# Performance work log

Measured on AMD Instinct MI355X. Metric: run time of the kernel, lower is better.

Reference implementation:

```python
import jax, jax.numpy as jnp
import numpy as np

B, H, S, Dh = 2, 16, 2048, 64


def setup_inputs() -> dict:
    key = jax.random.key(0)
    kq, kk, kv = jax.random.split(key, 3)
    query = jax.random.normal(kq, (B, H, S, Dh), dtype=jnp.float32)
    k = jax.random.normal(kk, (B, H, S, Dh), dtype=jnp.float32)
    value = jax.random.normal(kv, (B, H, S, Dh), dtype=jnp.float32)
    mask = jnp.zeros((1, 1, S, S), dtype=jnp.float32)
    return {"query": query, "key": k, "value": value, "mask": mask}


def reference(query, key, value, mask):
    # scores: [B,H,S,S]
    dk = jnp.asarray(key.shape[-1], dtype=query.dtype)
    logits = jnp.einsum("bhqd,bhkd->bhqk", query, key) / jnp.sqrt(dk)
    logits = logits + mask * (-1e9)
    attention_weights = jax.nn.softmax(logits, axis=-1)
    output = jnp.einsum("bhqk,bhkd->bhqd", attention_weights, value)
    return (output, attention_weights)
```

## Files before the change

### kernel.cpp

```cpp
#include <hip/hip_runtime.h>
#include <hip/hip_bf16.h>
#include <stdint.h>

typedef __bf16 bf16;
typedef __attribute__((ext_vector_type(8))) __bf16 bf16x8;
typedef __attribute__((ext_vector_type(4))) float f32x4;

constexpr int S   = 2048;
constexpr int DH  = 64;
constexpr int BQ  = 16;
constexpr int LDP = S + 8;

__global__ __launch_bounds__(256, 2)
void attn_fused(const float* __restrict__ Q, const float* __restrict__ K,
                const float* __restrict__ V, const float* __restrict__ Msk,
                float* __restrict__ Out, float* __restrict__ W)
{
    __shared__ bf16  P[BQ][LDP];
    __shared__ float rs[4][BQ];
    __shared__ float inv[BQ];

    const int tid  = threadIdx.x;
    const int lane = tid & 63;
    const int wave = tid >> 6;
    const int c    = lane & 15;
    const int g    = lane >> 4;

    const int swz = (blockIdx.x & 7) * 512 + (blockIdx.x >> 3);
    const int bh = swz >> 7;
    const int q0 = (swz & 127) * BQ;

    const float* Qb = Q + (size_t)bh * S * DH;
    const float* Kb = K + (size_t)bh * S * DH;
    const float* Vb = V + (size_t)bh * S * DH;

    bf16x8 qlo, qhi;
    {
        const float* qr = Qb + (size_t)(q0 + c) * DH + g * 8;
        f32x4 a0 = *(const f32x4*)(qr);
        f32x4 a1 = *(const f32x4*)(qr + 4);
        f32x4 b0 = *(const f32x4*)(qr + 32);
        f32x4 b1 = *(const f32x4*)(qr + 36);
        #pragma unroll
        for (int j = 0; j < 4; ++j) {
            qlo[j]     = (bf16)a0[j];  qlo[j + 4] = (bf16)a1[j];
            qhi[j]     = (bf16)b0[j];  qhi[j + 4] = (bf16)b1[j];
        }
    }

    float sums[4] = {0.f, 0.f, 0.f, 0.f};
    for (int i = 0; i < 16; ++i) {
        const int k0 = (wave * 2 + i * 8) * 16;
        const float* kr0 = Kb + (size_t)(k0 + c) * DH + g * 8;
        const float* kr1 = kr0 + (size_t)16 * DH;
        f32x4 a0 = *(const f32x4*)(kr0);
        f32x4 a1 = *(const f32x4*)(kr0 + 4);
        f32x4 b0 = *(const f32x4*)(kr0 + 32);
        f32x4 b1 = *(const f32x4*)(kr0 + 36);
        f32x4 a2 = *(const f32x4*)(kr1);
        f32x4 a3 = *(const f32x4*)(kr1 + 4);
        f32x4 b2 = *(const f32x4*)(kr1 + 32);
        f32x4 b3 = *(const f32x4*)(kr1 + 36);
        const float* mrow = Msk + (size_t)(q0 + g * 4) * S + k0 + c;
        float m0 = mrow[0], m1 = mrow[S], m2 = mrow[2 * S], m3 = mrow[3 * S];
        float n0 = mrow[16], n1 = mrow[S + 16], n2 = mrow[2 * S + 16], n3 = mrow[3 * S + 16];

        bf16x8 kl0, kh0, kl1, kh1;
        #pragma unroll
        for (int j = 0; j < 4; ++j) {
            kl0[j] = (bf16)a0[j];  kl0[j + 4] = (bf16)a1[j];
            kh0[j] = (bf16)b0[j];  kh0[j + 4] = (bf16)b1[j];
            kl1[j] = (bf16)a2[j];  kl1[j + 4] = (bf16)a3[j];
            kh1[j] = (bf16)b2[j];  kh1[j + 4] = (bf16)b3[j];
        }
        f32x4 acc0 = {0.f, 0.f, 0.f, 0.f};
        f32x4 acc1 = {0.f, 0.f, 0.f, 0.f};
        acc0 = __builtin_amdgcn_mfma_f32_16x16x32_bf16(qlo, kl0, acc0, 0, 0, 0);
        acc0 = __builtin_amdgcn_mfma_f32_16x16x32_bf16(qhi, kh0, acc0, 0, 0, 0);
        acc1 = __builtin_amdgcn_mfma_f32_16x16x32_bf16(qlo, kl1, acc1, 0, 0, 0);
        acc1 = __builtin_amdgcn_mfma_f32_16x16x32_bf16(qhi, kh1, acc1, 0, 0, 0);

        const float mk[4] = {m0, m1, m2, m3};
        const float nk[4] = {n0, n1, n2, n3};
        #pragma unroll
        for (int r = 0; r < 4; ++r) {
            const int row = g * 4 + r;
            const float p0 = __expf(acc0[r] * 0.125f + mk[r] * (-1e9f));
            const float p1 = __expf(acc1[r] * 0.125f + nk[r] * (-1e9f));
            sums[r] += p0 + p1;
            P[row][k0 + c]      = (bf16)p0;
            P[row][k0 + 16 + c] = (bf16)p1;
        }
    }

    #pragma unroll
    for (int r = 0; r < 4; ++r) {
        float s = sums[r];
        s += __shfl_xor(s, 1); s += __shfl_xor(s, 2);
        s += __shfl_xor(s, 4); s += __shfl_xor(s, 8);
        if (c == 0) rs[wave][g * 4 + r] = s;
    }
    __syncthreads();
    if (tid < BQ) inv[tid] = 1.f / (rs[0][tid] + rs[1][tid] + rs[2][tid] + rs[3][tid]);
    __syncthreads();

    float* Wb = W + (size_t)bh * S * S + (size_t)q0 * S;
    #pragma unroll
    for (int it = 0; it < (BQ * S) / (256 * 8); ++it) {
        const int flat = (it * 256 + tid) * 8;
        const int row  = flat >> 11;
        const int col  = flat & (S - 1);
        bf16x8 pv = *(const bf16x8*)&P[row][col];
        const float is = inv[row];
        float* dst = Wb + (size_t)row * S + col;
        f32x4 o0 = { (float)pv[0] * is, (float)pv[1] * is,
                     (float)pv[2] * is, (float)pv[3] * is };
        f32x4 o1 = { (float)pv[4] * is, (float)pv[5] * is,
                     (float)pv[6] * is, (float)pv[7] * is };
        *(f32x4*)(dst)     = o0;
        *(f32x4*)(dst + 4) = o1;
    }

    f32x4 oacc[4] = {{0,0,0,0},{0,0,0,0},{0,0,0,0},{0,0,0,0}};
    const int kbase = wave * (S / 4);
    for (int kc = 0; kc < 16; ++kc) {
        const int kb = kbase + kc * 32;
        bf16x8 pa = *(const bf16x8*)&P[c][kb + g * 8];
        const float* vp = Vb + (size_t)(kb + g * 8) * DH + c;
        float vv0[8], vv1[8], vv2[8], vv3[8];
        #pragma unroll
        for (int j = 0; j < 8; ++j) {
            const float* vr = vp + (size_t)j * DH;
            vv0[j] = vr[0];  vv1[j] = vr[16];
            vv2[j] = vr[32]; vv3[j] = vr[48];
        }
        bf16x8 vb0, vb1, vb2, vb3;
        #pragma unroll
        for (int j = 0; j < 8; ++j) {
            vb0[j] = (bf16)vv0[j]; vb1[j] = (bf16)vv1[j];
            vb2[j] = (bf16)vv2[j]; vb3[j] = (bf16)vv3[j];
        }
        oacc[0] = __builtin_amdgcn_mfma_f32_16x16x32_bf16(pa, vb0, oacc[0], 0, 0, 0);
        oacc[1] = __builtin_amdgcn_mfma_f32_16x16x32_bf16(pa, vb1, oacc[1], 0, 0, 0);
        oacc[2] = __builtin_amdgcn_mfma_f32_16x16x32_bf16(pa, vb2, oacc[2], 0, 0, 0);
        oacc[3] = __builtin_amdgcn_mfma_f32_16x16x32_bf16(pa, vb3, oacc[3], 0, 0, 0);
    }

    __syncthreads();
    float* opart = (float*)&P[0][0];
    #pragma unroll
    for (int d4 = 0; d4 < 4; ++d4)
        #pragma unroll
        for (int r = 0; r < 4; ++r)
            opart[wave * 1024 + (g * 4 + r) * 64 + d4 * 16 + c] = oacc[d4][r];
    __syncthreads();

    {
        const int q = tid >> 4;
        const int d = (tid & 15) * 4;
        const float* p0 = opart + q * 64 + d;
        f32x4 o = *(const f32x4*)(p0)
                + *(const f32x4*)(p0 + 1024)
                + *(const f32x4*)(p0 + 2048)
                + *(const f32x4*)(p0 + 3072);
        const float is = inv[q];
        o.x *= is; o.y *= is; o.z *= is; o.w *= is;
        float* Ob = Out + ((size_t)bh * S + q0 + q) * DH + d;
        *(f32x4*)Ob = o;
    }
}

extern "C" void kernel_launch(void* const* d_in, const int* in_sizes, int n_in,
                              void* d_out, int out_size, void* d_ws, size_t ws_size,
                              hipStream_t stream) {
    const float* Q   = (const float*)d_in[0];
    const float* K   = (const float*)d_in[1];
    const float* V   = (const float*)d_in[2];
    const float* Msk = (const float*)d_in[3];

    float* Out = (float*)d_out;
    float* W   = Out + (size_t)2 * 16 * 2048 * 64;

    dim3 grid(32 * (S / BQ));
    dim3 block(256);
    hipLaunchKernelGGL(attn_fused, grid, block, 0, stream, Q, K, V, Msk, Out, W);
}
```

Baseline: 408.7 us.

## Recompute QK^T in second pass instead of staging probabilities in LDS

Removes the 64KB shared-memory P buffer. The kernel now runs two passes over K: the first computes only the row sums of exp, and the second recomputes the scores, writes normalized weights directly to global memory with nontemporal stores, and feeds the bf16 probabilities straight into the PV MFMA from registers. The MFMA operand order is transposed so each lane holds one query row, which also lets the mask be read with vector loads. Lower LDS use permits higher occupancy (launch bounds raised to 4 blocks), at the cost of reading K twice and redoing the QK MFMAs and exp.

```diff
diff --git a/kernel.cpp b/kernel.cpp
--- a/kernel.cpp
+++ b/kernel.cpp
@@ -6,19 +6,19 @@
 typedef __attribute__((ext_vector_type(8))) __bf16 bf16x8;
 typedef __attribute__((ext_vector_type(4))) float f32x4;
 
-constexpr int S   = 2048;
-constexpr int DH  = 64;
-constexpr int BQ  = 16;
-constexpr int LDP = S + 8;
-
-__global__ __launch_bounds__(256, 2)
+constexpr int S  = 2048;
+constexpr int DH = 64;
+constexpr int BQ = 16;
+
+
+__global__ __launch_bounds__(256, 4)
 void attn_fused(const float* __restrict__ Q, const float* __restrict__ K,
                 const float* __restrict__ V, const float* __restrict__ Msk,
                 float* __restrict__ Out, float* __restrict__ W)
 {
-    __shared__ bf16  P[BQ][LDP];
     __shared__ float rs[4][BQ];
     __shared__ float inv[BQ];
+    __shared__ float opart[4][BQ][DH];
 
     const int tid  = threadIdx.x;
     const int lane = tid & 63;
@@ -48,9 +48,12 @@
         }
     }
 
-    float sums[4] = {0.f, 0.f, 0.f, 0.f};
-    for (int i = 0; i < 16; ++i) {
-        const int k0 = (wave * 2 + i * 8) * 16;
+    const int kbase = wave * (S / 4);
+    const float* mrow = Msk + (size_t)(q0 + c) * S;
+
+    float s = 0.f;
+    for (int kc = 0; kc < 16; ++kc) {
+        const int k0 = kbase + kc * 32;
         const float* kr0 = Kb + (size_t)(k0 + c) * DH + g * 8;
         const float* kr1 = kr0 + (size_t)16 * DH;
         f32x4 a0 = *(const f32x4*)(kr0);
@@ -61,9 +64,8 @@
         f32x4 a3 = *(const f32x4*)(kr1 + 4);
         f32x4 b2 = *(const f32x4*)(kr1 + 32);
         f32x4 b3 = *(const f32x4*)(kr1 + 36);
-        const float* mrow = Msk + (size_t)(q0 + g * 4) * S + k0 + c;
-        float m0 = mrow[0], m1 = mrow[S], m2 = mrow[2 * S], m3 = mrow[3 * S];
-        float n0 = mrow[16], n1 = mrow[S + 16], n2 = mrow[2 * S + 16], n3 = mrow[3 * S + 16];
+        f32x4 m0 = *(const f32x4*)(mrow + k0 + 4 * g);
+        f32x4 m1 = *(const f32x4*)(mrow + k0 + 16 + 4 * g);
 
         bf16x8 kl0, kh0, kl1, kh1;
         #pragma unroll
@@ -75,94 +77,111 @@
         }
         f32x4 acc0 = {0.f, 0.f, 0.f, 0.f};
         f32x4 acc1 = {0.f, 0.f, 0.f, 0.f};
-        acc0 = __builtin_amdgcn_mfma_f32_16x16x32_bf16(qlo, kl0, acc0, 0, 0, 0);
-        acc0 = __builtin_amdgcn_mfma_f32_16x16x32_bf16(qhi, kh0, acc0, 0, 0, 0);
-        acc1 = __builtin_amdgcn_mfma_f32_16x16x32_bf16(qlo, kl1, acc1, 0, 0, 0);
-        acc1 = __builtin_amdgcn_mfma_f32_16x16x32_bf16(qhi, kh1, acc1, 0, 0, 0);
-
-        const float mk[4] = {m0, m1, m2, m3};
-        const float nk[4] = {n0, n1, n2, n3};
+        acc0 = __builtin_amdgcn_mfma_f32_16x16x32_bf16(kl0, qlo, acc0, 0, 0, 0);
+        acc0 = __builtin_amdgcn_mfma_f32_16x16x32_bf16(kh0, qhi, acc0, 0, 0, 0);
+        acc1 = __builtin_amdgcn_mfma_f32_16x16x32_bf16(kl1, qlo, acc1, 0, 0, 0);
+        acc1 = __builtin_amdgcn_mfma_f32_16x16x32_bf16(kh1, qhi, acc1, 0, 0, 0);
         #pragma unroll
         for (int r = 0; r < 4; ++r) {
-            const int row = g * 4 + r;
-            const float p0 = __expf(acc0[r] * 0.125f + mk[r] * (-1e9f));
-            const float p1 = __expf(acc1[r] * 0.125f + nk[r] * (-1e9f));
-            sums[r] += p0 + p1;
-            P[row][k0 + c]      = (bf16)p0;
-            P[row][k0 + 16 + c] = (bf16)p1;
-        }
-    }
-
-    #pragma unroll
-    for (int r = 0; r < 4; ++r) {
-        float s = sums[r];
-        s += __shfl_xor(s, 1); s += __shfl_xor(s, 2);
-        s += __shfl_xor(s, 4); s += __shfl_xor(s, 8);
-        if (c == 0) rs[wave][g * 4 + r] = s;
-    }
+            s += __expf(acc0[r] * 0.125f + m0[r] * (-1e9f));
+            s += __expf(acc1[r] * 0.125f + m1[r] * (-1e9f));
+        }
+    }
+    s += __shfl_xor(s, 16);
+    s += __shfl_xor(s, 32);
+    if (lane < 16) rs[wave][lane] = s;
     __syncthreads();
     if (tid < BQ) inv[tid] = 1.f / (rs[0][tid] + rs[1][tid] + rs[2][tid] + rs[3][tid]);
     __syncthreads();
-
-    float* Wb = W + (size_t)bh * S * S + (size_t)q0 * S;
+    const float myinv = inv[c];
+
+    f32x4 oacc[4] = {{0,0,0,0},{0,0,0,0},{0,0,0,0},{0,0,0,0}};
+    float* Wrow = W + (size_t)bh * S * S + (size_t)(q0 + c) * S;
+
+    for (int kc = 0; kc < 16; ++kc) {
+        const int k0 = kbase + kc * 32;
+
+        const float* vp0 = Vb + (size_t)(k0 + 4 * g) * DH + c;
+        const float* vp1 = vp0 + (size_t)16 * DH;
+        float vv[4][8];
+        #pragma unroll
+        for (int j = 0; j < 4; ++j) {
+            #pragma unroll
+            for (int dt = 0; dt < 4; ++dt) {
+                vv[dt][j]     = vp0[j * DH + dt * 16];
+                vv[dt][j + 4] = vp1[j * DH + dt * 16];
+            }
+        }
+
+        const float* kr0 = Kb + (size_t)(k0 + c) * DH + g * 8;
+        const float* kr1 = kr0 + (size_t)16 * DH;
+        f32x4 a0 = *(const f32x4*)(kr0);
+        f32x4 a1 = *(const f32x4*)(kr0 + 4);
+        f32x4 b0 = *(const f32x4*)(kr0 + 32);
+        f32x4 b1 = *(const f32x4*)(kr0 + 36);
+        f32x4 a2 = *(const f32x4*)(kr1);
+        f32x4 a3 = *(const f32x4*)(kr1 + 4);
+        f32x4 b2 = *(const f32x4*)(kr1 + 32);
+        f32x4 b3 = *(const f32x4*)(kr1 + 36);
+        f32x4 m0 = *(const f32x4*)(mrow + k0 + 4 * g);
+        f32x4 m1 = *(const f32x4*)(mrow + k0 + 16 + 4 * g);
+
+        bf16x8 kl0, kh0, kl1, kh1;
+        #pragma unroll
+        for (int j = 0; j < 4; ++j) {
+            kl0[j] = (bf16)a0[j];  kl0[j + 4] = (bf16)a1[j];
+            kh0[j] = (bf16)b0[j];  kh0[j + 4] = (bf16)b1[j];
+            kl1[j] = (bf16)a2[j];  kl1[j + 4] = (bf16)a3[j];
+            kh1[j] = (bf16)b2[j];  kh1[j + 4] = (bf16)b3[j];
+        }
+        f32x4 acc0 = {0.f, 0.f, 0.f, 0.f};
+        f32x4 acc1 = {0.f, 0.f, 0.f, 0.f};
+        acc0 = __builtin_amdgcn_mfma_f32_16x16x32_bf16(kl0, qlo, acc0, 0, 0, 0);
+        acc0 = __builtin_amdgcn_mfma_f32_16x16x32_bf16(kh0, qhi, acc0, 0, 0, 0);
+        acc1 = __builtin_amdgcn_mfma_f32_16x16x32_bf16(kl1, qlo, acc1, 0, 0, 0);
+        acc1 = __builtin_amdgcn_mfma_f32_16x16x32_bf16(kh1, qhi, acc1, 0, 0, 0);
+
+        float p0[4], p1[4];
+        #pragma unroll
+        for (int r = 0; r < 4; ++r) {
+            p0[r] = __expf(acc0[r] * 0.125f + m0[r] * (-1e9f));
+            p1[r] = __expf(acc1[r] * 0.125f + m1[r] * (-1e9f));
+        }
+
+        f32x4 w0 = { p0[0] * myinv, p0[1] * myinv, p0[2] * myinv, p0[3] * myinv };
+        f32x4 w1 = { p1[0] * myinv, p1[1] * myinv, p1[2] * myinv, p1[3] * myinv };
+        __builtin_nontemporal_store(w0, (f32x4*)(Wrow + k0 + 4 * g));
+        __builtin_nontemporal_store(w1, (f32x4*)(Wrow + k0 + 16 + 4 * g));
+
+        bf16x8 pa;
+        #pragma unroll
+        for (int j = 0; j < 4; ++j) {
+            pa[j]     = (bf16)p0[j];
+            pa[j + 4] = (bf16)p1[j];
+        }
+        #pragma unroll
+        for (int dt = 0; dt < 4; ++dt) {
+            bf16x8 vb;
+            #pragma unroll
+            for (int j = 0; j < 8; ++j) vb[j] = (bf16)vv[dt][j];
+            oacc[dt] = __builtin_amdgcn_mfma_f32_16x16x32_bf16(pa, vb, oacc[dt], 0, 0, 0);
+        }
+    }
+
     #pragma unroll
-    for (int it = 0; it < (BQ * S) / (256 * 8); ++it) {
-        const int flat = (it * 256 + tid) * 8;
-        const int row  = flat >> 11;
-        const int col  = flat & (S - 1);
-        bf16x8 pv = *(const bf16x8*)&P[row][col];
-        const float is = inv[row];
-        float* dst = Wb + (size_t)row * S + col;
-        f32x4 o0 = { (float)pv[0] * is, (float)pv[1] * is,
-                     (float)pv[2] * is, (float)pv[3] * is };
-        f32x4 o1 = { (float)pv[4] * is, (float)pv[5] * is,
-                     (float)pv[6] * is, (float)pv[7] * is };
-        *(f32x4*)(dst)     = o0;
-        *(f32x4*)(dst + 4) = o1;
-    }
-
-    f32x4 oacc[4] = {{0,0,0,0},{0,0,0,0},{0,0,0,0},{0,0,0,0}};
-    const int kbase = wave * (S / 4);
-    for (int kc = 0; kc < 16; ++kc) {
-        const int kb = kbase + kc * 32;
-        bf16x8 pa = *(const bf16x8*)&P[c][kb + g * 8];
-        const float* vp = Vb + (size_t)(kb + g * 8) * DH + c;
-        float vv0[8], vv1[8], vv2[8], vv3[8];
-        #pragma unroll
-        for (int j = 0; j < 8; ++j) {
-            const float* vr = vp + (size_t)j * DH;
-            vv0[j] = vr[0];  vv1[j] = vr[16];
-            vv2[j] = vr[32]; vv3[j] = vr[48];
-        }
-        bf16x8 vb0, vb1, vb2, vb3;
-        #pragma unroll
-        for (int j = 0; j < 8; ++j) {
-            vb0[j] = (bf16)vv0[j]; vb1[j] = (bf16)vv1[j];
-            vb2[j] = (bf16)vv2[j]; vb3[j] = (bf16)vv3[j];
-        }
-        oacc[0] = __builtin_amdgcn_mfma_f32_16x16x32_bf16(pa, vb0, oacc[0], 0, 0, 0);
-        oacc[1] = __builtin_amdgcn_mfma_f32_16x16x32_bf16(pa, vb1, oacc[1], 0, 0, 0);
-        oacc[2] = __builtin_amdgcn_mfma_f32_16x16x32_bf16(pa, vb2, oacc[2], 0, 0, 0);
-        oacc[3] = __builtin_amdgcn_mfma_f32_16x16x32_bf16(pa, vb3, oacc[3], 0, 0, 0);
-    }
-
-    __syncthreads();
-    float* opart = (float*)&P[0][0];
-    #pragma unroll
-    for (int d4 = 0; d4 < 4; ++d4)
+    for (int dt = 0; dt < 4; ++dt)
         #pragma unroll
         for (int r = 0; r < 4; ++r)
-            opart[wave * 1024 + (g * 4 + r) * 64 + d4 * 16 + c] = oacc[d4][r];
+            opart[wave][4 * g + r][16 * dt + c] = oacc[dt][r];
     __syncthreads();
 
     {
         const int q = tid >> 4;
         const int d = (tid & 15) * 4;
-        const float* p0 = opart + q * 64 + d;
-        f32x4 o = *(const f32x4*)(p0)
-                + *(const f32x4*)(p0 + 1024)
-                + *(const f32x4*)(p0 + 2048)
-                + *(const f32x4*)(p0 + 3072);
+        f32x4 o = *(const f32x4*)&opart[0][q][d]
+                + *(const f32x4*)&opart[1][q][d]
+                + *(const f32x4*)&opart[2][q][d]
+                + *(const f32x4*)&opart[3][q][d];
         const float is = inv[q];
         o.x *= is; o.y *= is; o.z *= is; o.w *= is;
         float* Ob = Out + ((size_t)bh * S + q0 + q) * DH + d;
```

Result: slower. 657.4 us (+60.8%).
